# Kernel optimization log

Measured on AMD Instinct MI355X. Metric: run time of the kernel, lower is better.

Reference implementation:

```python
import jax, jax.numpy as jnp
import numpy as np

B, NX, NY, D_FEAT, CTX, S, T = 64, 32, 32, 1024, 512, 32, 4
N = NX * NY


def build_adjacency_matrix(nx, ny):
    # 4-neighborhood grid adjacency with self loops (faithful to original loop)
    adj = np.eye(nx * ny, dtype=np.float32)
    row = 0
    for i in range(nx):
        for j in range(ny):
            if i > 0:
                adj[row, j + (i - 1) * nx] = 1.0
            if i < nx - 1:
                adj[row, j + (i + 1) * nx] = 1.0
            if j > 0:
                adj[row, j - 1 + i * nx] = 1.0
            if j < ny - 1:
                adj[row, j + 1 + i * nx] = 1.0
            row += 1
    return adj


def setup_inputs() -> dict:
    key = jax.random.key(0)
    ks = jax.random.split(key, 12)
    s = 0.02
    return {
        "images": jax.random.normal(ks[0], (B, N, D_FEAT), jnp.float32),
        "q_encoding": jax.random.normal(ks[1], (B, CTX), jnp.float32),
        "lstm_outputs": jax.random.normal(ks[2], (B, S, CTX), jnp.float32),
        "q_length": jax.random.randint(ks[3], (B,), 1, S + 1, jnp.int32),
        "adj": jnp.asarray(build_adjacency_matrix(NX, NY)),
        "initKB_w": jax.random.normal(ks[4], (CTX, D_FEAT), jnp.float32) * s,
        "initKB_b": jnp.zeros((CTX,), jnp.float32),
        "W_w": jax.random.normal(ks[5], (CTX, 2 * CTX), jnp.float32) * s,
        "W_b": jnp.zeros((CTX,), jnp.float32),
        "qInput_w": jax.random.normal(ks[6], (CTX, CTX), jnp.float32) * s,
        "qInput_b": jnp.zeros((CTX,), jnp.float32),
        "qInputT_w": jax.random.normal(ks[7], (T, CTX, CTX), jnp.float32) * s,
        "qInputT_b": jnp.zeros((T, CTX), jnp.float32),
        "cmd_w": jax.random.normal(ks[8], (1, CTX), jnp.float32) * s,
        "cmd_b": jnp.zeros((1,), jnp.float32),
    }


def reference(images, q_encoding, lstm_outputs, q_length, adj,
              initKB_w, initKB_b, W_w, W_b, qInput_w, qInput_b,
              qInputT_w, qInputT_b, cmd_w, cmd_b) -> jnp.ndarray:
    n_iter = qInputT_w.shape[0]
    seq = lstm_outputs.shape[1]
    # loc_init: images [B,N,D_FEAT] -> x_loc [B,N,CTX]
    x_loc = jnp.einsum("bnd,cd->bnc", images, initKB_w) + initKB_b
    # shared first command layer (cfg.CMD_INPUT_ACT = elu)
    q1 = jax.nn.elu(q_encoding @ qInput_w.T + qInput_b)  # [B,CTX]
    valid = jnp.arange(seq)[None, :] < q_length[:, None]  # [B,S]
    for t in range(n_iter):
        # extract_textual_command
        q_cmd = q1 @ qInputT_w[t].T + qInputT_b[t]  # [B,CTX]
        raw_att = jnp.einsum("bsd,d->bs", q_cmd[:, None, :] * lstm_outputs, cmd_w[0]) + cmd_b[0]
        raw_att = jnp.where(valid, raw_att, -1e30)
        att = jax.nn.softmax(raw_att, axis=-1)  # [B,S]
        cmd = jnp.einsum("bs,bsd->bd", att, lstm_outputs)  # [B,CTX]
        # propagate_message: concat + linear, then dense adjacency matmul
        cmd_tiled = jnp.broadcast_to(cmd[:, None, :], x_loc.shape)
        support = jnp.concatenate([x_loc, cmd_tiled], axis=-1) @ W_w.T + W_b  # [B,N,CTX]
        x_new = jnp.einsum("nm,bmd->bnd", adj, support)  # [B,N,CTX]
        x_loc = jax.nn.elu(x_new) if t < n_iter - 1 else x_new
    return x_loc
```

## Files before the change

kernel.cpp:

```cpp
#include <hip/hip_runtime.h>
#include <math.h>

#define NB 64
#define NNODES 1024
#define CTXD 512
#define SEQL 32

typedef __attribute__((ext_vector_type(8))) short short8;
typedef __attribute__((ext_vector_type(4))) float floatx4;

__device__ __forceinline__ float bf2f(unsigned short u) {
  union { unsigned int i; float f; } v; v.i = ((unsigned int)u) << 16; return v.f;
}
__device__ __forceinline__ unsigned short f2bf(float f) {
  union { float f; unsigned int i; } v; v.f = f;
  unsigned int r = v.i + 0x7fffu + ((v.i >> 16) & 1u);
  return (unsigned short)(r >> 16);
}
__device__ __forceinline__ float elu1(float x) { return x > 0.f ? x : expm1f(x); }

__device__ __forceinline__ void gload16(const void* g, void* l) {
  __builtin_amdgcn_global_load_lds((const __attribute__((address_space(1))) void*)g,
                                   (__attribute__((address_space(3))) void*)l, 16, 0, 0);
}

__global__ __launch_bounds__(256) void pack_k(const float* __restrict__ kbw,
                                              const float* __restrict__ Ww,
                                              const float* __restrict__ qiw,
                                              const float* __restrict__ qtw,
                                              unsigned short* __restrict__ kb_bf,
                                              unsigned short* __restrict__ w1_bf,
                                              float* __restrict__ qiT,
                                              float* __restrict__ qTT,
                                              float* __restrict__ w2T) {
  int idx = blockIdx.x * 256 + threadIdx.x;
  if (idx < 524288) {
    kb_bf[idx] = f2bf(kbw[idx]);
  } else if (idx < 786432) {
    int o = idx - 524288;
    w1_bf[o] = f2bf(Ww[(o >> 9) * 1024 + (o & 511)]);
  } else if (idx < 1048576) {
    int o = idx - 786432;
    int k = o >> 9, c = o & 511;
    qiT[o] = qiw[c * 512 + k];
  } else if (idx < 2097152) {
    int o = idx - 1048576;
    int t = o >> 18, r = o & 262143;
    int k = r >> 9, c = r & 511;
    qTT[o] = qtw[((size_t)t * 512 + c) * 512 + k];
  } else {
    int o = idx - 2097152;
    int k = o >> 9, c = o & 511;
    w2T[o] = Ww[c * 1024 + 512 + k];
  }
}

__global__ __launch_bounds__(512) void q1_k(const float* __restrict__ q_enc,
                                            const float* __restrict__ qiT,
                                            const float* __restrict__ qInput_b,
                                            float* __restrict__ q1) {
  int b = blockIdx.x, c = threadIdx.x;
  __shared__ float qes[512];
  qes[c] = q_enc[b * 512 + c];
  __syncthreads();
  float a0 = qInput_b[c], a1 = 0.f, a2 = 0.f, a3 = 0.f;
#pragma unroll 4
  for (int k = 0; k < 512; k += 4) {
    a0 += qes[k] * qiT[k * 512 + c];
    a1 += qes[k + 1] * qiT[(k + 1) * 512 + c];
    a2 += qes[k + 2] * qiT[(k + 2) * 512 + c];
    a3 += qes[k + 3] * qiT[(k + 3) * 512 + c];
  }
  q1[b * 512 + c] = elu1(a0 + a1 + a2 + a3);
}

__global__ __launch_bounds__(512) void cmdt_k(
    const float* __restrict__ q1, const float* __restrict__ lstm,
    const int* __restrict__ q_len,
    const float* __restrict__ qTT, const float* __restrict__ qT_b,
    const float* __restrict__ cmd_w, const float* __restrict__ cmd_b,
    const float* __restrict__ w2T, const float* __restrict__ W_b,
    float* __restrict__ bias2) {
  int b = blockIdx.x & 63;
  int t = blockIdx.x >> 6;
  int c = threadIdx.x;
  __shared__ float q1s[512];
  __shared__ float us[512];
  __shared__ float red[512];
  __shared__ float atts[32];
  __shared__ float cmds[512];

  q1s[c] = q1[b * 512 + c];
  __syncthreads();

  const float* wt = qTT + (size_t)t * 262144;
  float a0 = qT_b[t * 512 + c], a1 = 0.f, a2 = 0.f, a3 = 0.f;
#pragma unroll 4
  for (int k = 0; k < 512; k += 4) {
    a0 += q1s[k] * wt[k * 512 + c];
    a1 += q1s[k + 1] * wt[(k + 1) * 512 + c];
    a2 += q1s[k + 2] * wt[(k + 2) * 512 + c];
    a3 += q1s[k + 3] * wt[(k + 3) * 512 + c];
  }
  us[c] = (a0 + a1 + a2 + a3) * cmd_w[c];
  __syncthreads();

  const float* lstmb = lstm + (size_t)b * SEQL * 512;
  {
    int s = c >> 4, u = c & 15;
    float p = 0.f;
    const float* lr = lstmb + s * 512;
    for (int r = u; r < 512; r += 16) p += us[r] * lr[r];
    red[c] = p;
  }
  __syncthreads();
  if (c < 32) {
    float raw = cmd_b[0];
    for (int u = 0; u < 16; u++) raw += red[c * 16 + u];
    raw = (c < q_len[b]) ? raw : -1e30f;
    float mx = raw;
    for (int off = 16; off; off >>= 1) mx = fmaxf(mx, __shfl_xor(mx, off, 32));
    float e = expf(raw - mx);
    float sm = e;
    for (int off = 16; off; off >>= 1) sm += __shfl_xor(sm, off, 32);
    atts[c] = e / sm;
  }
  __syncthreads();
  float cd = 0.f;
#pragma unroll
  for (int s = 0; s < 32; s++) cd += atts[s] * lstmb[s * 512 + c];
  cmds[c] = cd;
  __syncthreads();

  float b0 = W_b[c], b1 = 0.f, b2 = 0.f, b3 = 0.f;
#pragma unroll 4
  for (int k = 0; k < 512; k += 4) {
    b0 += cmds[k] * w2T[k * 512 + c];
    b1 += cmds[k + 1] * w2T[(k + 1) * 512 + c];
    b2 += cmds[k + 2] * w2T[(k + 2) * 512 + c];
    b3 += cmds[k + 3] * w2T[(k + 3) * 512 + c];
  }
  bias2[((size_t)(t * 64 + b)) * 512 + c] = b0 + b1 + b2 + b3;
}

__global__ __launch_bounds__(256) void stencil_k(const unsigned short* __restrict__ x,
                                                 unsigned short* __restrict__ y) {
  int g = blockIdx.x * 256 + threadIdx.x;
  int v = g & 63;
  int n = (g >> 6) & 1023;
  int b = g >> 16;
  size_t base = ((((size_t)b << 10) + n) << 9) + v * 8;
  const unsigned short* p = x + base;
  float acc[8];
  short8 s = *(const short8*)p;
#pragma unroll
  for (int j = 0; j < 8; j++) acc[j] = bf2f((unsigned short)s[j]);
  int i = n >> 5, jj = n & 31;
  if (i > 0) {
    short8 t = *(const short8*)(p - 32 * 512);
#pragma unroll
    for (int j = 0; j < 8; j++) acc[j] += bf2f((unsigned short)t[j]);
  }
  if (i < 31) {
    short8 t = *(const short8*)(p + 32 * 512);
#pragma unroll
    for (int j = 0; j < 8; j++) acc[j] += bf2f((unsigned short)t[j]);
  }
  if (jj > 0) {
    short8 t = *(const short8*)(p - 512);
#pragma unroll
    for (int j = 0; j < 8; j++) acc[j] += bf2f((unsigned short)t[j]);
  }
  if (jj < 31) {
    short8 t = *(const short8*)(p + 512);
#pragma unroll
    for (int j = 0; j < 8; j++) acc[j] += bf2f((unsigned short)t[j]);
  }
  short8 o;
#pragma unroll
  for (int j = 0; j < 8; j++) o[j] = (short)f2bf(acc[j]);
  *(short8*)(y + base) = o;
}

template <int AF32, int MODE>
__global__ __launch_bounds__(256) void gemm_bt(
    const void* __restrict__ Ap, int lda,
    const unsigned short* __restrict__ Bw, int ldb, int K,
    const float* __restrict__ cbias, const float* __restrict__ bias2,
    void* __restrict__ Cp) {
  constexpr int ABYTES = AF32 ? 16384 : 8192;
  __shared__ __align__(128) char smem[ABYTES + 8192];
  char* As = smem;
  char* Bs = smem + ABYTES;

  const int tid = threadIdx.x;
  const int lane = tid & 63;
  const int wave = tid >> 6;
  const int wr = (wave >> 1) * 64;
  const int wc = (wave & 1) * 64;
  const int lr = lane & 15;
  const int lk = lane >> 4;

  int bid = blockIdx.x;
  int cpx = gridDim.x >> 3;
  int wg = (bid & 7) * cpx + (bid >> 3);
  int mtile = wg >> 2;
  int ntile = wg & 3;
  const size_t rowBase = (size_t)mtile * 128;
  const int colBase = ntile * 128;

  floatx4 acc[4][4];
#pragma unroll
  for (int m = 0; m < 4; m++)
#pragma unroll
    for (int n = 0; n < 4; n++) acc[m][n] = {0.f, 0.f, 0.f, 0.f};

  for (int k0 = 0; k0 < K; k0 += 32) {
    __syncthreads();
    if constexpr (AF32) {
      const float* A = (const float*)Ap;
#pragma unroll
      for (int i = 0; i < 4; i++) {
        int g = tid + i * 256;
        gload16(A + (rowBase + (g >> 3)) * (size_t)lda + k0 + (g & 7) * 4, As + g * 16);
      }
    } else {
      const unsigned short* A = (const unsigned short*)Ap;
#pragma unroll
      for (int i = 0; i < 2; i++) {
        int g = tid + i * 256;
        gload16(A + (rowBase + (g >> 2)) * (size_t)lda + k0 + (g & 3) * 8, As + g * 16);
      }
    }
#pragma unroll
    for (int i = 0; i < 2; i++) {
      int g = tid + i * 256;
      gload16(Bw + (size_t)(colBase + (g >> 2)) * ldb + k0 + (g & 3) * 8, Bs + g * 16);
    }
    __syncthreads();

    short8 a[4], b[4];
    if constexpr (AF32) {
#pragma unroll
      for (int m = 0; m < 4; m++) {
        const float* p = (const float*)As + (wr + m * 16 + lr) * 32 + lk * 8;
        short8 t;
#pragma unroll
        for (int j = 0; j < 8; j++) t[j] = (short)f2bf(p[j]);
        a[m] = t;
      }
    } else {
#pragma unroll
      for (int m = 0; m < 4; m++)
        a[m] = *(const short8*)((const unsigned short*)As + (wr + m * 16 + lr) * 32 + lk * 8);
    }
#pragma unroll
    for (int n = 0; n < 4; n++)
      b[n] = *(const short8*)((const unsigned short*)Bs + (wc + n * 16 + lr) * 32 + lk * 8);

#pragma unroll
    for (int m = 0; m < 4; m++)
#pragma unroll
      for (int n = 0; n < 4; n++)
        acc[m][n] = __builtin_amdgcn_mfma_f32_16x16x32_bf16(a[m], b[n], acc[m][n], 0, 0, 0);
  }

#pragma unroll
  for (int m = 0; m < 4; m++) {
#pragma unroll
    for (int q = 0; q < 4; q++) {
      size_t grow = rowBase + wr + m * 16 + lk * 4 + q;
      float degf = 0.f;
      const float* b2 = nullptr;
      if constexpr (MODE != 0) {
        int nsp = (int)(grow & 1023);
        int ii = nsp >> 5, jj = nsp & 31;
        degf = (float)(1 + (ii > 0) + (ii < 31) + (jj > 0) + (jj < 31));
        b2 = bias2 + (grow >> 10) * CTXD;
      }
#pragma unroll
      for (int n = 0; n < 4; n++) {
        int gcol = colBase + wc + n * 16 + lr;
        float v = acc[m][n][q];
        if constexpr (MODE == 0) v += cbias[gcol];
        else v += degf * b2[gcol];
        if constexpr (MODE == 1) v = elu1(v);
        if constexpr (MODE == 2) ((float*)Cp)[grow * CTXD + gcol] = v;
        else ((unsigned short*)Cp)[grow * CTXD + gcol] = f2bf(v);
      }
    }
  }
}

extern "C" void kernel_launch(void* const* d_in, const int* in_sizes, int n_in,
                              void* d_out, int out_size, void* d_ws, size_t ws_size,
                              hipStream_t stream) {
  const float* images   = (const float*)d_in[0];
  const float* q_enc    = (const float*)d_in[1];
  const float* lstm     = (const float*)d_in[2];
  const int*   q_len    = (const int*)d_in[3];
  const float* initKB_w = (const float*)d_in[5];
  const float* initKB_b = (const float*)d_in[6];
  const float* W_w      = (const float*)d_in[7];
  const float* W_b      = (const float*)d_in[8];
  const float* qInput_w = (const float*)d_in[9];
  const float* qInput_b = (const float*)d_in[10];
  const float* qT_w     = (const float*)d_in[11];
  const float* qT_b     = (const float*)d_in[12];
  const float* cmd_w    = (const float*)d_in[13];
  const float* cmd_b    = (const float*)d_in[14];

  char* ws = (char*)d_ws;
  unsigned short* y     = (unsigned short*)ws;
  float*          qiT   = (float*)ws;
  float*          qTT   = (float*)(ws + 1048576);
  float*          w2T   = (float*)(ws + 5242880);
  unsigned short* kb_bf = (unsigned short*)(ws + 67108864);
  unsigned short* w1_bf = (unsigned short*)(ws + 68157440);
  float*          bias2 = (float*)(ws + 68681728);
  float*          q1    = (float*)(ws + 69206016);
  unsigned short* xloc  = (unsigned short*)d_out;

  pack_k<<<9216, 256, 0, stream>>>(initKB_w, W_w, qInput_w, qT_w,
                                   kb_bf, w1_bf, qiT, qTT, w2T);
  q1_k<<<64, 512, 0, stream>>>(q_enc, qiT, qInput_b, q1);
  cmdt_k<<<256, 512, 0, stream>>>(q1, lstm, q_len, qTT, qT_b, cmd_w, cmd_b,
                                  w2T, W_b, bias2);

  gemm_bt<1, 0><<<2048, 256, 0, stream>>>(images, 1024, kb_bf, 1024, 1024,
                                          initKB_b, nullptr, xloc);

  for (int t = 0; t < 4; t++) {
    stencil_k<<<16384, 256, 0, stream>>>(xloc, y);
    if (t < 3)
      gemm_bt<0, 1><<<2048, 256, 0, stream>>>(y, 512, w1_bf, 512, 512,
                                              nullptr, bias2 + (size_t)t * 64 * 512, xloc);
    else
      gemm_bt<0, 2><<<2048, 256, 0, stream>>>(y, 512, w1_bf, 512, 512,
                                              nullptr, bias2 + (size_t)t * 64 * 512, d_out);
  }
}
```

Baseline: 625.7 us.

## Double GEMM K-tile to 64, XOR-swizzle LDS, convert fp32 A to bf16 before LDS

Each k-step of the MFMA GEMM now covers 64 instead of 32, which halves the number of barrier pairs per output tile. Both LDS tiles use an XOR swizzle on 16-byte chunks to avoid bank conflicts when reading rows for MFMA. The fp32 A path now loads through registers and converts to bf16 before the LDS store, so LDS holds bf16 and there is no per-read conversion. The cost is that those fp32 loads become synchronous register loads instead of async global_load_lds.

```diff
diff --git a/kernel.cpp b/kernel.cpp
--- a/kernel.cpp
+++ b/kernel.cpp
@@ -1,4 +1,5 @@
 #include <hip/hip_runtime.h>
+#include <hip/hip_bf16.h>
 #include <math.h>
 
 #define NB 64
@@ -188,10 +189,8 @@
     const unsigned short* __restrict__ Bw, int ldb, int K,
     const float* __restrict__ cbias, const float* __restrict__ bias2,
     void* __restrict__ Cp) {
-  constexpr int ABYTES = AF32 ? 16384 : 8192;
-  __shared__ __align__(128) char smem[ABYTES + 8192];
-  char* As = smem;
-  char* Bs = smem + ABYTES;
+  __shared__ __align__(128) unsigned short As[128 * 64];
+  __shared__ __align__(128) unsigned short Bs[128 * 64];
 
   const int tid = threadIdx.x;
   const int lane = tid & 63;
@@ -200,6 +199,7 @@
   const int wc = (wave & 1) * 64;
   const int lr = lane & 15;
   const int lk = lane >> 4;
+  const int lr7 = lr & 7;
 
   int bid = blockIdx.x;
   int cpx = gridDim.x >> 3;
@@ -215,54 +215,62 @@
 #pragma unroll
     for (int n = 0; n < 4; n++) acc[m][n] = {0.f, 0.f, 0.f, 0.f};
 
-  for (int k0 = 0; k0 < K; k0 += 32) {
+  for (int k0 = 0; k0 < K; k0 += 64) {
     __syncthreads();
     if constexpr (AF32) {
       const float* A = (const float*)Ap;
 #pragma unroll
-      for (int i = 0; i < 4; i++) {
-        int g = tid + i * 256;
-        gload16(A + (rowBase + (g >> 3)) * (size_t)lda + k0 + (g & 7) * 4, As + g * 16);
+      for (int j = 0; j < 4; j++) {
+        int g = j * 256 + tid;
+        int r = g >> 3, s = g & 7;
+        const float* src = A + (rowBase + r) * (size_t)lda + k0 + s * 8;
+        floatx4 v0 = *(const floatx4*)src;
+        floatx4 v1 = *(const floatx4*)(src + 4);
+        short8 t;
+#pragma unroll
+        for (int e = 0; e < 4; e++) {
+          __hip_bfloat16 h0 = __float2bfloat16(v0[e]);
+          __hip_bfloat16 h1 = __float2bfloat16(v1[e]);
+          t[e] = (short)*reinterpret_cast<unsigned short*>(&h0);
+          t[e + 4] = (short)*reinterpret_cast<unsigned short*>(&h1);
+        }
+        *(short8*)((char*)As + r * 128 + ((s ^ (r & 7)) << 4)) = t;
       }
     } else {
       const unsigned short* A = (const unsigned short*)Ap;
 #pragma unroll
-      for (int i = 0; i < 2; i++) {
-        int g = tid + i * 256;
-        gload16(A + (rowBase + (g >> 2)) * (size_t)lda + k0 + (g & 3) * 8, As + g * 16);
+      for (int j = 0; j < 4; j++) {
+        int g = j * 256 + tid;
+        int r = g >> 3, u = g & 7;
+        gload16(A + (rowBase + r) * (size_t)lda + k0 + ((u ^ (r & 7)) << 3),
+                (char*)As + g * 16);
       }
     }
 #pragma unroll
-    for (int i = 0; i < 2; i++) {
-      int g = tid + i * 256;
-      gload16(Bw + (size_t)(colBase + (g >> 2)) * ldb + k0 + (g & 3) * 8, Bs + g * 16);
+    for (int j = 0; j < 4; j++) {
+      int g = j * 256 + tid;
+      int r = g >> 3, u = g & 7;
+      gload16(Bw + (size_t)(colBase + r) * ldb + k0 + ((u ^ (r & 7)) << 3),
+              (char*)Bs + g * 16);
     }
     __syncthreads();
 
-    short8 a[4], b[4];
-    if constexpr (AF32) {
-#pragma unroll
-      for (int m = 0; m < 4; m++) {
-        const float* p = (const float*)As + (wr + m * 16 + lr) * 32 + lk * 8;
-        short8 t;
-#pragma unroll
-        for (int j = 0; j < 8; j++) t[j] = (short)f2bf(p[j]);
-        a[m] = t;
-      }
-    } else {
+#pragma unroll
+    for (int kk = 0; kk < 2; kk++) {
+      const int ub = ((kk << 2) + lk) ^ lr7;
+      short8 a[4], b[4];
 #pragma unroll
       for (int m = 0; m < 4; m++)
-        a[m] = *(const short8*)((const unsigned short*)As + (wr + m * 16 + lr) * 32 + lk * 8);
+        a[m] = *(const short8*)((const char*)As + (wr + m * 16 + lr) * 128 + (ub << 4));
+#pragma unroll
+      for (int n = 0; n < 4; n++)
+        b[n] = *(const short8*)((const char*)Bs + (wc + n * 16 + lr) * 128 + (ub << 4));
+#pragma unroll
+      for (int m = 0; m < 4; m++)
+#pragma unroll
+        for (int n = 0; n < 4; n++)
+          acc[m][n] = __builtin_amdgcn_mfma_f32_16x16x32_bf16(a[m], b[n], acc[m][n], 0, 0, 0);
     }
-#pragma unroll
-    for (int n = 0; n < 4; n++)
-      b[n] = *(const short8*)((const unsigned short*)Bs + (wc + n * 16 + lr) * 32 + lk * 8);
-
-#pragma unroll
-    for (int m = 0; m < 4; m++)
-#pragma unroll
-      for (int n = 0; n < 4; n++)
-        acc[m][n] = __builtin_amdgcn_mfma_f32_16x16x32_bf16(a[m], b[n], acc[m][n], 0, 0, 0);
   }
 
 #pragma unroll
```

After: 544.3 us. -13.0%, faster.

## Double-buffer GEMM LDS tiles with XOR swizzle and register-staged fp32 A conversion

Applied to the files above, without the earlier changes.

Rewrites the bf16 MFMA GEMM main loop to ping-pong between two LDS buffers, so global loads for the next K slice are issued before compute on the current one. LDS rows are XOR-swizzled to avoid bank conflicts on the short8 fragment reads. For fp32 A inputs, data is now loaded into registers and converted to bf16 once before being written to LDS, instead of being converted from fp32 LDS on every fragment read. This adds register pressure and doubles the LDS footprint for bf16 inputs, and the loop assumes K is a multiple of 64.

```diff
diff --git a/kernel.cpp b/kernel.cpp
--- a/kernel.cpp
+++ b/kernel.cpp
@@ -1,4 +1,5 @@
 #include <hip/hip_runtime.h>
+#include <hip/hip_bf16.h>
 #include <math.h>
 
 #define NB 64
@@ -188,10 +189,10 @@
     const unsigned short* __restrict__ Bw, int ldb, int K,
     const float* __restrict__ cbias, const float* __restrict__ bias2,
     void* __restrict__ Cp) {
-  constexpr int ABYTES = AF32 ? 16384 : 8192;
-  __shared__ __align__(128) char smem[ABYTES + 8192];
-  char* As = smem;
-  char* Bs = smem + ABYTES;
+  __shared__ __align__(128) unsigned short As0[128 * 32];
+  __shared__ __align__(128) unsigned short As1[128 * 32];
+  __shared__ __align__(128) unsigned short Bs0[128 * 32];
+  __shared__ __align__(128) unsigned short Bs1[128 * 32];
 
   const int tid = threadIdx.x;
   const int lane = tid & 63;
@@ -209,60 +210,105 @@
   const size_t rowBase = (size_t)mtile * 128;
   const int colBase = ntile * 128;
 
+  const int g0 = tid, g1 = 256 + tid;
+  const int r0 = g0 >> 2, u0 = g0 & 3, su0 = (u0 ^ (r0 & 3));
+  const int r1 = g1 >> 2, u1 = g1 & 3, su1 = (u1 ^ (r1 & 3));
+  const int ub = lk ^ (lr & 3);
+
   floatx4 acc[4][4];
 #pragma unroll
   for (int m = 0; m < 4; m++)
 #pragma unroll
     for (int n = 0; n < 4; n++) acc[m][n] = {0.f, 0.f, 0.f, 0.f};
 
-  for (int k0 = 0; k0 < K; k0 += 32) {
-    __syncthreads();
+  const unsigned short* Abf = (const unsigned short*)Ap;
+  const float* Af = (const float*)Ap;
+
+  auto stageB = [&](unsigned short* Bsb, int k0) {
+    gload16(Bw + (size_t)(colBase + r0) * ldb + k0 + (su0 << 3), (char*)Bsb + g0 * 16);
+    gload16(Bw + (size_t)(colBase + r1) * ldb + k0 + (su1 << 3), (char*)Bsb + g1 * 16);
+  };
+  auto stageAbf = [&](unsigned short* Asb, int k0) {
+    gload16(Abf + (rowBase + r0) * (size_t)lda + k0 + (su0 << 3), (char*)Asb + g0 * 16);
+    gload16(Abf + (rowBase + r1) * (size_t)lda + k0 + (su1 << 3), (char*)Asb + g1 * 16);
+  };
+  auto loadA32 = [&](int k0, floatx4* v) {
+    const float* s0 = Af + (rowBase + r0) * (size_t)lda + k0 + u0 * 8;
+    const float* s1 = Af + (rowBase + r1) * (size_t)lda + k0 + u1 * 8;
+    v[0] = *(const floatx4*)s0;
+    v[1] = *(const floatx4*)(s0 + 4);
+    v[2] = *(const floatx4*)s1;
+    v[3] = *(const floatx4*)(s1 + 4);
+  };
+  auto writeA32 = [&](unsigned short* Asb, const floatx4* v) {
+    short8 t0, t1;
+#pragma unroll
+    for (int e = 0; e < 4; e++) {
+      t0[e] = (short)f2bf(v[0][e]);
+      t0[e + 4] = (short)f2bf(v[1][e]);
+      t1[e] = (short)f2bf(v[2][e]);
+      t1[e + 4] = (short)f2bf(v[3][e]);
+    }
+    *(short8*)((char*)Asb + r0 * 64 + (su0 << 4)) = t0;
+    *(short8*)((char*)Asb + r1 * 64 + (su1 << 4)) = t1;
+  };
+  auto compute = [&](const unsigned short* Asb, const unsigned short* Bsb) {
+    short8 a[4], b[4];
+#pragma unroll
+    for (int m = 0; m < 4; m++)
+      a[m] = *(const short8*)((const char*)Asb + (wr + m * 16 + lr) * 64 + (ub << 4));
+#pragma unroll
+    for (int n = 0; n < 4; n++)
+      b[n] = *(const short8*)((const char*)Bsb + (wc + n * 16 + lr) * 64 + (ub << 4));
+#pragma unroll
+    for (int m = 0; m < 4; m++)
+#pragma unroll
+      for (int n = 0; n < 4; n++)
+        acc[m][n] = __builtin_amdgcn_mfma_f32_16x16x32_bf16(a[m], b[n], acc[m][n], 0, 0, 0);
+  };
+
+  if constexpr (AF32) {
+    floatx4 va[4];
+    loadA32(0, va);
+    stageB(Bs0, 0);
+    writeA32(As0, va);
+  } else {
+    stageAbf(As0, 0);
+    stageB(Bs0, 0);
+  }
+  __syncthreads();
+
+  for (int k0 = 0; k0 < K; k0 += 64) {
     if constexpr (AF32) {
-      const float* A = (const float*)Ap;
-#pragma unroll
-      for (int i = 0; i < 4; i++) {
-        int g = tid + i * 256;
-        gload16(A + (rowBase + (g >> 3)) * (size_t)lda + k0 + (g & 7) * 4, As + g * 16);
-      }
+      floatx4 va[4];
+      loadA32(k0 + 32, va);
+      stageB(Bs1, k0 + 32);
+      compute(As0, Bs0);
+      writeA32(As1, va);
     } else {
-      const unsigned short* A = (const unsigned short*)Ap;
-#pragma unroll
-      for (int i = 0; i < 2; i++) {
-        int g = tid + i * 256;
-        gload16(A + (rowBase + (g >> 2)) * (size_t)lda + k0 + (g & 3) * 8, As + g * 16);
-      }
-    }
-#pragma unroll
-    for (int i = 0; i < 2; i++) {
-      int g = tid + i * 256;
-      gload16(Bw + (size_t)(colBase + (g >> 2)) * ldb + k0 + (g & 3) * 8, Bs + g * 16);
+      stageAbf(As1, k0 + 32);
+      stageB(Bs1, k0 + 32);
+      compute(As0, Bs0);
     }
     __syncthreads();
 
-    short8 a[4], b[4];
+    bool more = (k0 + 64) < K;
     if constexpr (AF32) {
-#pragma unroll
-      for (int m = 0; m < 4; m++) {
-        const float* p = (const float*)As + (wr + m * 16 + lr) * 32 + lk * 8;
-        short8 t;
-#pragma unroll
-        for (int j = 0; j < 8; j++) t[j] = (short)f2bf(p[j]);
-        a[m] = t;
+      floatx4 va[4];
+      if (more) {
+        loadA32(k0 + 64, va);
+        stageB(Bs0, k0 + 64);
       }
+      compute(As1, Bs1);
+      if (more) writeA32(As0, va);
     } else {
-#pragma unroll
-      for (int m = 0; m < 4; m++)
-        a[m] = *(const short8*)((const unsigned short*)As + (wr + m * 16 + lr) * 32 + lk * 8);
+      if (more) {
+        stageAbf(As0, k0 + 64);
+        stageB(Bs0, k0 + 64);
+      }
+      compute(As1, Bs1);
     }
-#pragma unroll
-    for (int n = 0; n < 4; n++)
-      b[n] = *(const short8*)((const unsigned short*)Bs + (wc + n * 16 + lr) * 32 + lk * 8);
-
-#pragma unroll
-    for (int m = 0; m < 4; m++)
-#pragma unroll
-      for (int n = 0; n < 4; n++)
-        acc[m][n] = __builtin_amdgcn_mfma_f32_16x16x32_bf16(a[m], b[n], acc[m][n], 0, 0, 0);
+    __syncthreads();
   }
 
 #pragma unroll
```

Measured after the change: 588.3 us. 6.0% less time.
